# Kernel tuning notes

Measured on AMD Instinct MI355X. Metric: run time of the kernel, lower is better.

The kernel has to match this reference:

```python
import jax, jax.numpy as jnp
import numpy as np

TOP_K = 4
NUM_EXPERTS = 32
HIDDEN = 2880


def setup_inputs() -> dict:
    key = jax.random.key(0)
    k1, k2, k3 = jax.random.split(key, 3)
    hidden_states = jax.random.normal(k1, (4, 4096, HIDDEN), dtype=jnp.float32)
    # Router params: weight [num_experts, hidden], bias [num_experts]
    weight = jax.random.normal(k2, (NUM_EXPERTS, HIDDEN), dtype=jnp.float32) * (1.0 / np.sqrt(HIDDEN))
    bias = jax.random.normal(k3, (NUM_EXPERTS,), dtype=jnp.float32) * 0.01
    return {"hidden_states": hidden_states, "weight": weight, "bias": bias}


def reference(hidden_states, weight, bias):
    # Flatten tokens: [T, H]
    h = hidden_states.reshape(-1, hidden_states.shape[-1])
    # Router logits: F.linear(h, W, b) = h @ W.T + b -> [T, E]
    router_logits = jnp.einsum("th,eh->te", h, weight) + bias
    # Top-k over experts
    router_top_value, router_indices = jax.lax.top_k(router_logits, TOP_K)  # [T, K]
    # Softmax over the k selected logits (in float32, cast back)
    router_top_value = jax.nn.softmax(router_top_value.astype(jnp.float32), axis=-1).astype(router_logits.dtype)
    # Scatter into dense zero scores: [T, E]
    router_scores = jnp.zeros_like(router_logits)
    t_idx = jnp.arange(h.shape[0])[:, None]  # [T, 1] broadcast against [T, K]
    router_scores = router_scores.at[t_idx, router_indices].set(router_top_value)
    return router_scores, router_indices
```

## Files before the change

kernel.cpp:

```cpp
#include <hip/hip_runtime.h>
#include <math.h>

#define NE 32
#define HID 2880
#define NSTEP 90
#define TT 64
#define THREADS 256
#define WSB_BYTES (3 * NSTEP * 2 * 64 * 16)

typedef short bf16x8 __attribute__((ext_vector_type(8)));
typedef float f32x4 __attribute__((ext_vector_type(4)));

union FragU { uint4 q; bf16x8 v; };

#define GLL(gsrc, ldst)                                                        \
  __builtin_amdgcn_global_load_lds(                                            \
      (const __attribute__((address_space(1))) unsigned int*)(gsrc),           \
      (__attribute__((address_space(3))) unsigned int*)(ldst), 16, 0, 0)

__global__ void __launch_bounds__(256) wsplit_kernel(
    const float* __restrict__ w, unsigned int* __restrict__ wsB)
{
  const int gid = blockIdx.x * 256 + threadIdx.x;
  const int s  = gid >> 7;
  const int tl = (gid >> 6) & 1;
  const int l  = gid & 63;

  const float* src = w + (size_t)(tl * 16 + (l & 15)) * HID + s * 32 + ((l >> 4) * 8);
  float4 xa = *(const float4*)src;
  float4 xb = *(const float4*)(src + 4);
  float x[8] = {xa.x, xa.y, xa.z, xa.w, xb.x, xb.y, xb.z, xb.w};

  unsigned int u0[8], u1[8], u2[8];
#pragma unroll
  for (int j = 0; j < 8; ++j) {
    unsigned int ux = __float_as_uint(x[j]);
    u0[j] = ux & 0xFFFF0000u;
    float r1 = x[j] - __uint_as_float(u0[j]);
    u1[j] = __float_as_uint(r1) & 0xFFFF0000u;
    float r2 = r1 - __uint_as_float(u1[j]);
    u2[j] = __float_as_uint(r2);
  }

  uint4* dst = (uint4*)wsB;
  uint4 d;
  d.x = __builtin_amdgcn_perm(u0[1], u0[0], 0x07060302u);
  d.y = __builtin_amdgcn_perm(u0[3], u0[2], 0x07060302u);
  d.z = __builtin_amdgcn_perm(u0[5], u0[4], 0x07060302u);
  d.w = __builtin_amdgcn_perm(u0[7], u0[6], 0x07060302u);
  dst[((0 * NSTEP + s) * 2 + tl) * 64 + l] = d;
  d.x = __builtin_amdgcn_perm(u1[1], u1[0], 0x07060302u);
  d.y = __builtin_amdgcn_perm(u1[3], u1[2], 0x07060302u);
  d.z = __builtin_amdgcn_perm(u1[5], u1[4], 0x07060302u);
  d.w = __builtin_amdgcn_perm(u1[7], u1[6], 0x07060302u);
  dst[((1 * NSTEP + s) * 2 + tl) * 64 + l] = d;
  d.x = __builtin_amdgcn_perm(u2[1], u2[0], 0x07060302u);
  d.y = __builtin_amdgcn_perm(u2[3], u2[2], 0x07060302u);
  d.z = __builtin_amdgcn_perm(u2[5], u2[4], 0x07060302u);
  d.w = __builtin_amdgcn_perm(u2[7], u2[6], 0x07060302u);
  dst[((2 * NSTEP + s) * 2 + tl) * 64 + l] = d;
}

__global__ void __launch_bounds__(THREADS, 4) router_mfma(
    const float* __restrict__ hs,
    const unsigned int* __restrict__ wsB,
    float* __restrict__ wsp,
    int T, int KQ, int ntg)
{
  __shared__ float smem[2][TT * 64];

  const int tid = threadIdx.x;
  const int wv  = __builtin_amdgcn_readfirstlane(tid >> 6);
  const int l   = tid & 63;
  const int q   = l >> 4;
  const int r15 = l & 15;
  const int tg  = blockIdx.x % ntg;
  const int kq  = blockIdx.x / ntg;
  const int t0  = tg * TT;

  int nsteps, s0;
  if (KQ == 4) { nsteps = (kq == 0) ? 24 : 22; s0 = (kq == 0) ? 0 : (2 + 22 * kq); }
  else         { nsteps = (kq == 0) ? 46 : 44; s0 = (kq == 0) ? 0 : 46; }
  const int nchunk = nsteps >> 1;

  int goff[4];
#pragma unroll
  for (int i = 0; i < 4; ++i) {
    int f = tid + 256 * i;
    int row = f >> 4;
    int G = (f & 15) ^ (row & 15);
    goff[i] = row * HID + G * 4;
  }

  const int hrowb = (wv * 16 + r15) * 256;

  f32x4 acc0 = {0.f, 0.f, 0.f, 0.f};
  f32x4 acc1 = {0.f, 0.f, 0.f, 0.f};

  const float* hbase = hs + (size_t)t0 * HID + s0 * 32;

#pragma unroll
  for (int i = 0; i < 4; ++i)
    GLL(hbase + goff[i], (char*)smem + (tid + 256 * i) * 16);
  __syncthreads();

#pragma clang loop unroll(disable)
  for (int c = 0; c < nchunk; ++c) {
    if (c + 1 < nchunk) {
      const float* hn = hbase + (c + 1) * 64;
      char* bn = (char*)smem + ((c + 1) & 1) * 16384;
#pragma unroll
      for (int i = 0; i < 4; ++i)
        GLL(hn + goff[i], bn + (tid + 256 * i) * 16);
    }
    const char* cb = (const char*)smem + (c & 1) * 16384;

#pragma unroll
    for (int sl = 0; sl < 2; ++sl) {
      const int sg = s0 + c * 2 + sl;

      const uint4* wb = (const uint4*)wsB;
      FragU W00, W01, W10, W11, W20, W21;
      W00.q = wb[((0 * NSTEP + sg) * 2 + 0) * 64 + l];
      W01.q = wb[((0 * NSTEP + sg) * 2 + 1) * 64 + l];
      W10.q = wb[((1 * NSTEP + sg) * 2 + 0) * 64 + l];
      W11.q = wb[((1 * NSTEP + sg) * 2 + 1) * 64 + l];
      W20.q = wb[((2 * NSTEP + sg) * 2 + 0) * 64 + l];
      W21.q = wb[((2 * NSTEP + sg) * 2 + 1) * 64 + l];

      float4 h0 = *(const float4*)(cb + hrowb + (((sl * 8 + 2 * q + 0) ^ r15) << 4));
      float4 h1 = *(const float4*)(cb + hrowb + (((sl * 8 + 2 * q + 1) ^ r15) << 4));
      float x[8] = {h0.x, h0.y, h0.z, h0.w, h1.x, h1.y, h1.z, h1.w};

      unsigned int u0[8], u1[8], u2[8];
#pragma unroll
      for (int j = 0; j < 8; ++j) {
        unsigned int ux = __float_as_uint(x[j]);
        u0[j] = ux & 0xFFFF0000u;
        float r1 = x[j] - __uint_as_float(u0[j]);
        u1[j] = __float_as_uint(r1) & 0xFFFF0000u;
        float r2 = r1 - __uint_as_float(u1[j]);
        u2[j] = __float_as_uint(r2);
      }
      FragU A0, A1, A2;
      A0.q.x = __builtin_amdgcn_perm(u0[1], u0[0], 0x07060302u);
      A0.q.y = __builtin_amdgcn_perm(u0[3], u0[2], 0x07060302u);
      A0.q.z = __builtin_amdgcn_perm(u0[5], u0[4], 0x07060302u);
      A0.q.w = __builtin_amdgcn_perm(u0[7], u0[6], 0x07060302u);
      A1.q.x = __builtin_amdgcn_perm(u1[1], u1[0], 0x07060302u);
      A1.q.y = __builtin_amdgcn_perm(u1[3], u1[2], 0x07060302u);
      A1.q.z = __builtin_amdgcn_perm(u1[5], u1[4], 0x07060302u);
      A1.q.w = __builtin_amdgcn_perm(u1[7], u1[6], 0x07060302u);
      A2.q.x = __builtin_amdgcn_perm(u2[1], u2[0], 0x07060302u);
      A2.q.y = __builtin_amdgcn_perm(u2[3], u2[2], 0x07060302u);
      A2.q.z = __builtin_amdgcn_perm(u2[5], u2[4], 0x07060302u);
      A2.q.w = __builtin_amdgcn_perm(u2[7], u2[6], 0x07060302u);

      acc0 = __builtin_amdgcn_mfma_f32_16x16x32_bf16(A0.v, W00.v, acc0, 0, 0, 0);
      acc0 = __builtin_amdgcn_mfma_f32_16x16x32_bf16(A0.v, W10.v, acc0, 0, 0, 0);
      acc0 = __builtin_amdgcn_mfma_f32_16x16x32_bf16(A1.v, W00.v, acc0, 0, 0, 0);
      acc0 = __builtin_amdgcn_mfma_f32_16x16x32_bf16(A1.v, W10.v, acc0, 0, 0, 0);
      acc0 = __builtin_amdgcn_mfma_f32_16x16x32_bf16(A0.v, W20.v, acc0, 0, 0, 0);
      acc0 = __builtin_amdgcn_mfma_f32_16x16x32_bf16(A2.v, W00.v, acc0, 0, 0, 0);
      acc1 = __builtin_amdgcn_mfma_f32_16x16x32_bf16(A0.v, W01.v, acc1, 0, 0, 0);
      acc1 = __builtin_amdgcn_mfma_f32_16x16x32_bf16(A0.v, W11.v, acc1, 0, 0, 0);
      acc1 = __builtin_amdgcn_mfma_f32_16x16x32_bf16(A1.v, W01.v, acc1, 0, 0, 0);
      acc1 = __builtin_amdgcn_mfma_f32_16x16x32_bf16(A1.v, W11.v, acc1, 0, 0, 0);
      acc1 = __builtin_amdgcn_mfma_f32_16x16x32_bf16(A0.v, W21.v, acc1, 0, 0, 0);
      acc1 = __builtin_amdgcn_mfma_f32_16x16x32_bf16(A2.v, W01.v, acc1, 0, 0, 0);
    }
    __syncthreads();
  }

  float* dst = wsp + ((size_t)kq * T + t0 + wv * 16) * NE;
#pragma unroll
  for (int r = 0; r < 4; ++r) {
    dst[(q * 4 + r) * NE + r15]      = acc0[r];
    dst[(q * 4 + r) * NE + 16 + r15] = acc1[r];
  }
}

__global__ void __launch_bounds__(256) router_topk(
    const float* __restrict__ wsp, const float* __restrict__ bias,
    float* __restrict__ out, int T, int KQ)
{
  const int tok = blockIdx.x * 256 + threadIdx.x;

  float lg[NE];
#pragma unroll
  for (int e = 0; e < NE; e += 4) {
    float4 bb = *(const float4*)(bias + e);
    lg[e] = bb.x; lg[e+1] = bb.y; lg[e+2] = bb.z; lg[e+3] = bb.w;
  }
  for (int qq = 0; qq < KQ; ++qq) {
    const float* p = wsp + ((size_t)qq * T + tok) * NE;
#pragma unroll
    for (int e = 0; e < NE; e += 4) {
      float4 v = *(const float4*)(p + e);
      lg[e] += v.x; lg[e+1] += v.y; lg[e+2] += v.z; lg[e+3] += v.w;
    }
  }

  float tv[4]; int ti[4];
#pragma unroll
  for (int kk = 0; kk < 4; ++kk) {
    float m = -INFINITY; int mi = 0;
#pragma unroll
    for (int e = 0; e < NE; ++e) {
      bool gt = lg[e] > m;
      m  = gt ? lg[e] : m;
      mi = gt ? e : mi;
    }
    tv[kk] = m; ti[kk] = mi;
#pragma unroll
    for (int e = 0; e < NE; ++e)
      lg[e] = (e == mi) ? -INFINITY : lg[e];
  }

  float e1 = __expf(tv[1] - tv[0]);
  float e2 = __expf(tv[2] - tv[0]);
  float e3 = __expf(tv[3] - tv[0]);
  float inv = 1.0f / (1.0f + e1 + e2 + e3);
  float pr[4] = {inv, e1 * inv, e2 * inv, e3 * inv};

  float* orow = out + (size_t)tok * NE;
#pragma unroll
  for (int g = 0; g < 8; ++g) {
    float4 v;
    float* vp = (float*)&v;
#pragma unroll
    for (int cb = 0; cb < 4; ++cb) {
      int e = g * 4 + cb;
      float xx = 0.f;
      xx = (e == ti[0]) ? pr[0] : xx;
      xx = (e == ti[1]) ? pr[1] : xx;
      xx = (e == ti[2]) ? pr[2] : xx;
      xx = (e == ti[3]) ? pr[3] : xx;
      vp[cb] = xx;
    }
    *(float4*)(orow + g * 4) = v;
  }
  float* oidx = out + (size_t)T * NE + (size_t)tok * 4;
  float4 iv;
  iv.x = (float)ti[0]; iv.y = (float)ti[1]; iv.z = (float)ti[2]; iv.w = (float)ti[3];
  *(float4*)oidx = iv;
}

extern "C" void kernel_launch(void* const* d_in, const int* in_sizes, int n_in,
                              void* d_out, int out_size, void* d_ws, size_t ws_size,
                              hipStream_t stream) {
  const float* hs   = (const float*)d_in[0];
  const float* w    = (const float*)d_in[1];
  const float* bias = (const float*)d_in[2];
  float* out        = (float*)d_out;

  unsigned int* wsB = (unsigned int*)d_ws;
  float* wsp        = (float*)((char*)d_ws + WSB_BYTES);

  const int T   = in_sizes[0] / HID;
  const int ntg = T / TT;

  const size_t per_kq = (size_t)T * NE * 4;
  const int KQ = (ws_size >= WSB_BYTES + 4 * per_kq) ? 4 : 2;

  hipLaunchKernelGGL(wsplit_kernel, dim3(45), dim3(256), 0, stream, w, wsB);
  hipLaunchKernelGGL(router_mfma, dim3(ntg * KQ), dim3(THREADS), 0, stream,
                     hs, wsB, wsp, T, KQ, ntg);
  hipLaunchKernelGGL(router_topk, dim3(T / 256), dim3(256), 0, stream,
                     wsp, bias, out, T, KQ);
}
```

Before: 52.56 us.

## Stage router weight fragments through LDS alongside hidden states with explicit vmcnt waits

The per-chunk weight fragments now travel through a second double-buffered LDS region via global_load_lds, where before each wave read them straight from global memory inside the MFMA loop. Synchronization changes from a full __syncthreads to raw s_barrier plus a partial vmcnt(7) wait, so the prefetch of chunk c+1 stays in flight while chunk c is consumed. The occupancy hint is dropped from launch_bounds. The goal is to take global weight-load latency off the MFMA critical path and overlap it with compute, at the cost of extra LDS use (about 56KB per block) that may lower occupancy.

```diff
diff --git a/kernel.cpp b/kernel.cpp
--- a/kernel.cpp
+++ b/kernel.cpp
@@ -61,13 +61,14 @@
   dst[((2 * NSTEP + s) * 2 + tl) * 64 + l] = d;
 }
 
-__global__ void __launch_bounds__(THREADS, 4) router_mfma(
+__global__ void __launch_bounds__(THREADS) router_mfma(
     const float* __restrict__ hs,
     const unsigned int* __restrict__ wsB,
     float* __restrict__ wsp,
     int T, int KQ, int ntg)
 {
-  __shared__ float smem[2][TT * 64];
+  __shared__ float hbuf[2][4096];
+  __shared__ float wbuf[2][3072];
 
   const int tid = threadIdx.x;
   const int wv  = __builtin_amdgcn_readfirstlane(tid >> 6);
@@ -83,13 +84,21 @@
   else         { nsteps = (kq == 0) ? 46 : 44; s0 = (kq == 0) ? 0 : 46; }
   const int nchunk = nsteps >> 1;
 
-  int goff[4];
+  int goffH[4];
 #pragma unroll
   for (int i = 0; i < 4; ++i) {
     int f = tid + 256 * i;
     int row = f >> 4;
     int G = (f & 15) ^ (row & 15);
-    goff[i] = row * HID + G * 4;
+    goffH[i] = row * HID + G * 4;
+  }
+  int goffW[3];
+#pragma unroll
+  for (int i = 0; i < 3; ++i) {
+    int j = tid + 256 * i;
+    int f = j >> 6, e = j & 63;
+    int p = f >> 2, sl = (f >> 1) & 1, t = f & 1;
+    goffW[i] = ((p * 2 * NSTEP + sl * 2 + t) * 64 + e);
   }
 
   const int hrowb = (wv * 16 + r15) * 256;
@@ -98,35 +107,50 @@
   f32x4 acc1 = {0.f, 0.f, 0.f, 0.f};
 
   const float* hbase = hs + (size_t)t0 * HID + s0 * 32;
-
-#pragma unroll
-  for (int i = 0; i < 4; ++i)
-    GLL(hbase + goff[i], (char*)smem + (tid + 256 * i) * 16);
-  __syncthreads();
+  const uint4* wsb4 = (const uint4*)wsB;
+
+#define STAGE(j)                                                               \
+  {                                                                            \
+    const float* hn = hbase + (j) * 64;                                        \
+    char* hb_n = (char*)&hbuf[(j) & 1][0];                                     \
+    char* wb_n = (char*)&wbuf[(j) & 1][0];                                     \
+    _Pragma("unroll")                                                          \
+    for (int i = 0; i < 4; ++i)                                                \
+      GLL(hn + goffH[i], hb_n + (tid + 256 * i) * 16);                         \
+    _Pragma("unroll")                                                          \
+    for (int i = 0; i < 3; ++i)                                                \
+      GLL(wsb4 + goffW[i] + (size_t)(s0 + 2 * (j)) * 128,                      \
+          wb_n + (tid + 256 * i) * 16);                                        \
+  }
+
+  STAGE(0);
 
 #pragma clang loop unroll(disable)
   for (int c = 0; c < nchunk; ++c) {
+    __builtin_amdgcn_s_barrier();
+
     if (c + 1 < nchunk) {
-      const float* hn = hbase + (c + 1) * 64;
-      char* bn = (char*)smem + ((c + 1) & 1) * 16384;
-#pragma unroll
-      for (int i = 0; i < 4; ++i)
-        GLL(hn + goff[i], bn + (tid + 256 * i) * 16);
-    }
-    const char* cb = (const char*)smem + (c & 1) * 16384;
+      STAGE(c + 1);
+      asm volatile("s_waitcnt vmcnt(7)" ::: "memory");
+    } else {
+      asm volatile("s_waitcnt vmcnt(0)" ::: "memory");
+    }
+    __builtin_amdgcn_sched_barrier(0);
+    __builtin_amdgcn_s_barrier();
+    __builtin_amdgcn_sched_barrier(0);
+
+    const char* cb = (const char*)&hbuf[c & 1][0];
+    const uint4* wl = (const uint4*)&wbuf[c & 1][0];
 
 #pragma unroll
     for (int sl = 0; sl < 2; ++sl) {
-      const int sg = s0 + c * 2 + sl;
-
-      const uint4* wb = (const uint4*)wsB;
       FragU W00, W01, W10, W11, W20, W21;
-      W00.q = wb[((0 * NSTEP + sg) * 2 + 0) * 64 + l];
-      W01.q = wb[((0 * NSTEP + sg) * 2 + 1) * 64 + l];
-      W10.q = wb[((1 * NSTEP + sg) * 2 + 0) * 64 + l];
-      W11.q = wb[((1 * NSTEP + sg) * 2 + 1) * 64 + l];
-      W20.q = wb[((2 * NSTEP + sg) * 2 + 0) * 64 + l];
-      W21.q = wb[((2 * NSTEP + sg) * 2 + 1) * 64 + l];
+      W00.q = wl[(0 + sl * 2 + 0) * 64 + l];
+      W01.q = wl[(0 + sl * 2 + 1) * 64 + l];
+      W10.q = wl[(4 + sl * 2 + 0) * 64 + l];
+      W11.q = wl[(4 + sl * 2 + 1) * 64 + l];
+      W20.q = wl[(8 + sl * 2 + 0) * 64 + l];
+      W21.q = wl[(8 + sl * 2 + 1) * 64 + l];
 
       float4 h0 = *(const float4*)(cb + hrowb + (((sl * 8 + 2 * q + 0) ^ r15) << 4));
       float4 h1 = *(const float4*)(cb + hrowb + (((sl * 8 + 2 * q + 1) ^ r15) << 4));
@@ -169,7 +193,6 @@
       acc1 = __builtin_amdgcn_mfma_f32_16x16x32_bf16(A0.v, W21.v, acc1, 0, 0, 0);
       acc1 = __builtin_amdgcn_mfma_f32_16x16x32_bf16(A2.v, W01.v, acc1, 0, 0, 0);
     }
-    __syncthreads();
   }
 
   float* dst = wsp + ((size_t)kq * T + t0 + wv * 16) * NE;
```

Result: faster. 50.37 us (median of 2 runs) (-4.2%).
